# Performance work log

Hardware: AMD Instinct MI355X
Metric: run time of the kernel (lower is better)

## Reference

```python
import jax, jax.numpy as jnp
import numpy as np
from jax import lax

S, B, IN, H, L = 256, 8192, 1, 32, 2


def setup_inputs() -> dict:
    key = jax.random.key(0)
    ks = jax.random.split(key, 12)
    s = 1.0 / np.sqrt(H)
    return {
        "x": jax.random.normal(ks[0], (S, B, IN), dtype=jnp.float32),
        "h": jax.random.normal(ks[1], (L, B, H), dtype=jnp.float32),
        "W_ih0": jax.random.uniform(ks[2], (3 * H, IN), jnp.float32, -s, s),
        "W_hh0": jax.random.uniform(ks[3], (3 * H, H), jnp.float32, -s, s),
        "b_ih0": jax.random.uniform(ks[4], (3 * H,), jnp.float32, -s, s),
        "b_hh0": jax.random.uniform(ks[5], (3 * H,), jnp.float32, -s, s),
        "W_ih1": jax.random.uniform(ks[6], (3 * H, H), jnp.float32, -s, s),
        "W_hh1": jax.random.uniform(ks[7], (3 * H, H), jnp.float32, -s, s),
        "b_ih1": jax.random.uniform(ks[8], (3 * H,), jnp.float32, -s, s),
        "b_hh1": jax.random.uniform(ks[9], (3 * H,), jnp.float32, -s, s),
        "W_out": jax.random.uniform(ks[10], (1, H), jnp.float32, -s, s),
        "b_out": jax.random.uniform(ks[11], (1,), jnp.float32, -s, s),
    }


def _gru_layer(x_seq, h0, W_ih, W_hh, b_ih, b_hh):
    # x_seq: (S, B, D_in), h0: (B, H). PyTorch GRU gate math.
    def step(h, x_t):
        gi = x_t @ W_ih.T + b_ih            # (B, 3H)
        gh = h @ W_hh.T + b_hh              # (B, 3H)
        i_r, i_z, i_n = jnp.split(gi, 3, axis=-1)
        h_r, h_z, h_n = jnp.split(gh, 3, axis=-1)
        r = jax.nn.sigmoid(i_r + h_r)
        z = jax.nn.sigmoid(i_z + h_z)
        n = jnp.tanh(i_n + r * h_n)
        h_new = (1.0 - z) * n + z * h
        return h_new, h_new

    h_last, out = lax.scan(step, h0, x_seq)
    return out, h_last


def reference(x, h, W_ih0, W_hh0, b_ih0, b_hh0, W_ih1, W_hh1, b_ih1, b_hh1, W_out, b_out):
    out0, hl0 = _gru_layer(x, h[0], W_ih0, W_hh0, b_ih0, b_hh0)
    out1, hl1 = _gru_layer(out0, h[1], W_ih1, W_hh1, b_ih1, b_hh1)
    # per-timestep Linear loop == one batched matmul over (S, B, H)
    y = out1 @ W_out.T + b_out              # (S, B, 1)
    h_state = jnp.stack([hl0, hl1], axis=0)  # (L, B, H)
    return (y, h_state)
```

## Files before the change

kernel.cpp:

```cpp
#include <hip/hip_runtime.h>


#define S_LEN 256
#define B_SZ  8192
#define H_SZ  32
#define RS    40

typedef __attribute__((ext_vector_type(8))) short short8;
typedef __attribute__((ext_vector_type(4))) float f32x4;

#define MFMA(a, b, c) __builtin_amdgcn_mfma_f32_16x16x32_bf16(a, b, c, 0, 0, 0)

#if __has_builtin(__builtin_amdgcn_exp2f)
#define EXP2F(x) __builtin_amdgcn_exp2f(x)
#else
#define EXP2F(x) exp2f(x)
#endif
#if __has_builtin(__builtin_amdgcn_rcpf)
#define RCPF(x) __builtin_amdgcn_rcpf(x)
#else
#define RCPF(x) (1.0f / (x))
#endif

__device__ __forceinline__ float sigm_pre(float p) {
    return RCPF(1.0f + EXP2F(p));
}
__device__ __forceinline__ float tanh_pre(float p) {
    return 1.0f - 2.0f * RCPF(1.0f + EXP2F(p));
}

__device__ __forceinline__ unsigned short bf_rne1(float f) {
    union { float f; unsigned u; } x; x.f = f;
    unsigned u = x.u + 0x7fffu + ((x.u >> 16) & 1u);
    return (unsigned short)(u >> 16);
}

#if __has_builtin(__builtin_amdgcn_cvt_pk_bf16_f32)
typedef __bf16 bf16x2 __attribute__((ext_vector_type(2)));
__device__ __forceinline__ unsigned pk2(float a, float b) {
    union { bf16x2 v; unsigned u; } c;
    c.v = __builtin_amdgcn_cvt_pk_bf16_f32(a, b);
    return c.u;
}
#else
__device__ __forceinline__ unsigned pk2(float a, float b) {
    return (unsigned)bf_rne1(a) | ((unsigned)bf_rne1(b) << 16);
}
#endif

union Frag { short8 s8; unsigned u[4]; };

__global__ __launch_bounds__(256) void gru_bf(
    const float* __restrict__ x,
    const float* __restrict__ h_in,
    const float* __restrict__ W_ih0,
    const float* __restrict__ W_hh0,
    const float* __restrict__ b_ih0,
    const float* __restrict__ b_hh0,
    const float* __restrict__ W_ih1,
    const float* __restrict__ W_hh1,
    const float* __restrict__ b_ih1,
    const float* __restrict__ b_hh1,
    const float* __restrict__ W_out,
    const float* __restrict__ b_out,
    float* __restrict__ out)
{
    __shared__ __align__(16) float sx[S_LEN * 16];
    __shared__ __align__(16) float sy[2][S_LEN * 16];
    __shared__ __align__(16) unsigned short sh0s[3][16 * RS];
    __shared__ __align__(16) unsigned short sh1s[3][16 * RS];

    const int tid  = threadIdx.x;
    const int w    = tid >> 6;
    const int lane = tid & 63;
    const int n    = lane & 15;
    const int q    = lane >> 4;
    const int base = blockIdx.x * 16;
    const int bn   = base + n;
    const int wl   = w & 1;

    for (int s = tid; s < S_LEN * 4; s += 256) {
        const int t = s >> 2, c = s & 3;
        *(float4*)&sx[t * 16 + c * 4] = *(const float4*)&x[t * B_SZ + base + c * 4];
    }

    const float SRZ = -1.4426950408889634f;
    const float SN  =  2.8853900817779268f;

    short8 A_h[3], A_i[3];
    f32x4  C_h[3], C_i3;
    float  wi0r[4], wi0z[4], wi0n[4], bi0n[4];
    float  wo[4];
    float  hd[4];

    if (w < 2) {
#pragma unroll
        for (int t = 0; t < 3; ++t) {
            const float sc = (t < 2) ? SRZ : SN;
            const int row = 32 * t + 16 * wl + n;
#pragma unroll
            for (int e = 0; e < 8; ++e)
                A_h[t][e] = (short)bf_rne1(W_hh0[row * H_SZ + q * 8 + e] * sc);
#pragma unroll
            for (int r = 0; r < 4; ++r) {
                const int g = 32 * t + 16 * wl + 4 * q + r;
                C_h[t][r] = (t < 2) ? SRZ * (b_ih0[g] + b_hh0[g])
                                    : SN * b_hh0[g];
            }
        }
#pragma unroll
        for (int r = 0; r < 4; ++r) {
            const int j = 16 * wl + 4 * q + r;
            wi0r[r] = SRZ * W_ih0[j];
            wi0z[r] = SRZ * W_ih0[32 + j];
            wi0n[r] = SN  * W_ih0[64 + j];
            bi0n[r] = SN  * b_ih0[64 + j];
            hd[r]   = h_in[bn * H_SZ + j];
            wo[r]   = 0.f;
        }
    } else {
#pragma unroll
        for (int t = 0; t < 3; ++t) {
            const float sc = (t < 2) ? SRZ : SN;
            const int row = 32 * t + 16 * wl + n;
#pragma unroll
            for (int e = 0; e < 8; ++e) {
                A_h[t][e] = (short)bf_rne1(W_hh1[row * H_SZ + q * 8 + e] * sc);
                A_i[t][e] = (short)bf_rne1(W_ih1[row * H_SZ + q * 8 + e] * sc);
            }
#pragma unroll
            for (int r = 0; r < 4; ++r) {
                const int g = 32 * t + 16 * wl + 4 * q + r;
                C_h[t][r] = (t < 2) ? SRZ * (b_ih1[g] + b_hh1[g])
                                    : SN * b_hh1[g];
                if (t == 2) C_i3[r] = SN * b_ih1[g];
            }
        }
#pragma unroll
        for (int r = 0; r < 4; ++r) {
            const int j = 16 * wl + 4 * q + r;
            hd[r] = h_in[B_SZ * H_SZ + bn * H_SZ + j];
            wo[r] = W_out[j];
        }
    }
    const f32x4 Z4 = {0.f, 0.f, 0.f, 0.f};
    const float bout = b_out[0];

    short8 B0, B1;
    {
        Frag f;
        const float4 a = *(const float4*)&h_in[bn * H_SZ + q * 8];
        const float4 b = *(const float4*)&h_in[bn * H_SZ + q * 8 + 4];
        f.u[0] = pk2(a.x, a.y); f.u[1] = pk2(a.z, a.w);
        f.u[2] = pk2(b.x, b.y); f.u[3] = pk2(b.z, b.w);
        B0 = f.s8;
        const float4 c = *(const float4*)&h_in[B_SZ * H_SZ + bn * H_SZ + q * 8];
        const float4 d = *(const float4*)&h_in[B_SZ * H_SZ + bn * H_SZ + q * 8 + 4];
        f.u[0] = pk2(c.x, c.y); f.u[1] = pk2(c.z, c.w);
        f.u[2] = pk2(d.x, d.y); f.u[3] = pk2(d.z, d.w);
        B1 = f.s8;
    }

    __syncthreads();

    int buf = 0;
#pragma unroll 1
    for (int i = 0; i <= S_LEN; ++i) {
        if (w < 2) {
            if (i < S_LEN) {
                const float xc = sx[i * 16 + n];
                const f32x4 g0r = MFMA(A_h[0], B0, C_h[0]);
                const f32x4 g0z = MFMA(A_h[1], B0, C_h[1]);
                const f32x4 g0n = MFMA(A_h[2], B0, C_h[2]);
                float hv4[4];
#pragma unroll
                for (int r = 0; r < 4; ++r) {
                    const float rg = sigm_pre(fmaf(xc, wi0r[r], g0r[r]));
                    const float zg = sigm_pre(fmaf(xc, wi0z[r], g0z[r]));
                    const float ng = tanh_pre(fmaf(rg, g0n[r],
                                                   fmaf(xc, wi0n[r], bi0n[r])));
                    const float hv = fmaf(zg, hd[r] - ng, ng);
                    hd[r] = hv;
                    hv4[r] = hv;
                }
                *(uint2*)&sh0s[buf][n * RS + 16 * wl + 4 * q] =
                    make_uint2(pk2(hv4[0], hv4[1]), pk2(hv4[2], hv4[3]));
            }
        } else {
            if (i > 0) {
                const f32x4 ur = MFMA(A_h[0], B1, C_h[0]);
                const f32x4 uz = MFMA(A_h[1], B1, C_h[1]);
                const f32x4 un = MFMA(A_h[2], B1, C_h[2]);
                const f32x4 vr = MFMA(A_i[0], B0, Z4);
                const f32x4 vz = MFMA(A_i[1], B0, Z4);
                const f32x4 vn = MFMA(A_i[2], B0, C_i3);
                float hv4[4];
                float ys = 0.f;
#pragma unroll
                for (int r = 0; r < 4; ++r) {
                    const float rg = sigm_pre(ur[r] + vr[r]);
                    const float zg = sigm_pre(uz[r] + vz[r]);
                    const float ng = tanh_pre(fmaf(rg, un[r], vn[r]));
                    const float hv = fmaf(zg, hd[r] - ng, ng);
                    hd[r] = hv;
                    hv4[r] = hv;
                    ys = fmaf(hv, wo[r], ys);
                }
                *(uint2*)&sh1s[buf][n * RS + 16 * wl + 4 * q] =
                    make_uint2(pk2(hv4[0], hv4[1]), pk2(hv4[2], hv4[3]));
                ys += __shfl_xor(ys, 16);
                ys += __shfl_xor(ys, 32);
                if (lane < 16) sy[wl][(i - 1) * 16 + n] = ys;
            }
        }

        __syncthreads();

        if (i < S_LEN)
            B0 = *(const short8*)&sh0s[buf][n * RS + q * 8];
        if (w >= 2 && i > 0)
            B1 = *(const short8*)&sh1s[buf][n * RS + q * 8];

        buf = (buf == 2) ? 0 : buf + 1;
    }

    __syncthreads();

    for (int s = tid; s < S_LEN * 4; s += 256) {
        const int t = s >> 2, c = s & 3;
        const float4 a = *(const float4*)&sy[0][t * 16 + c * 4];
        const float4 b = *(const float4*)&sy[1][t * 16 + c * 4];
        *(float4*)&out[t * B_SZ + base + c * 4] =
            make_float4(a.x + b.x + bout, a.y + b.y + bout,
                        a.z + b.z + bout, a.w + b.w + bout);
    }

    const int j = 16 * wl + 4 * q;
    if (w < 2)
        *(float4*)&out[S_LEN * B_SZ + bn * H_SZ + j] =
            make_float4(hd[0], hd[1], hd[2], hd[3]);
    else
        *(float4*)&out[S_LEN * B_SZ + B_SZ * H_SZ + bn * H_SZ + j] =
            make_float4(hd[0], hd[1], hd[2], hd[3]);
}

extern "C" void kernel_launch(void* const* d_in, const int* in_sizes, int n_in,
                              void* d_out, int out_size, void* d_ws, size_t ws_size,
                              hipStream_t stream) {
    (void)in_sizes; (void)n_in; (void)out_size; (void)d_ws; (void)ws_size;
    const float* x     = (const float*)d_in[0];
    const float* h_in  = (const float*)d_in[1];
    const float* W_ih0 = (const float*)d_in[2];
    const float* W_hh0 = (const float*)d_in[3];
    const float* b_ih0 = (const float*)d_in[4];
    const float* b_hh0 = (const float*)d_in[5];
    const float* W_ih1 = (const float*)d_in[6];
    const float* W_hh1 = (const float*)d_in[7];
    const float* b_ih1 = (const float*)d_in[8];
    const float* b_hh1 = (const float*)d_in[9];
    const float* W_out = (const float*)d_in[10];
    const float* b_out = (const float*)d_in[11];

    dim3 grid(B_SZ / 16);
    dim3 block(256);
    gru_bf<<<grid, block, 0, stream>>>(x, h_in, W_ih0, W_hh0, b_ih0, b_hh0,
                                       W_ih1, W_hh1, b_ih1, b_hh1,
                                       W_out, b_out, (float*)d_out);
}
```

Before: 269.0 us.

## Double-buffer hidden state and compute output projection from shared bf16 state

```diff
diff --git a/kernel.cpp b/kernel.cpp
--- a/kernel.cpp
+++ b/kernel.cpp
@@ -48,9 +48,11 @@
 }
 #endif
 
-union Frag { short8 s8; unsigned u[4]; };
-
-__global__ __launch_bounds__(256) void gru_bf(
+__device__ __forceinline__ float bits_f(unsigned u) {
+    union { unsigned u; float f; } x; x.u = u; return x.f;
+}
+
+__global__ __launch_bounds__(256) void gru_lag(
     const float* __restrict__ x,
     const float* __restrict__ h_in,
     const float* __restrict__ W_ih0,
@@ -65,10 +67,10 @@
     const float* __restrict__ b_out,
     float* __restrict__ out)
 {
+    __shared__ __align__(16) unsigned short sh0[2][16 * RS];
+    __shared__ __align__(16) unsigned short sh1[2][16 * RS];
     __shared__ __align__(16) float sx[S_LEN * 16];
-    __shared__ __align__(16) float sy[2][S_LEN * 16];
-    __shared__ __align__(16) unsigned short sh0s[3][16 * RS];
-    __shared__ __align__(16) unsigned short sh1s[3][16 * RS];
+    __shared__ __align__(16) float sy[S_LEN * 16];
 
     const int tid  = threadIdx.x;
     const int w    = tid >> 6;
@@ -90,7 +92,7 @@
     short8 A_h[3], A_i[3];
     f32x4  C_h[3], C_i3;
     float  wi0r[4], wi0z[4], wi0n[4], bi0n[4];
-    float  wo[4];
+    float  wo8[8];
     float  hd[4];
 
     if (w < 2) {
@@ -116,7 +118,6 @@
             wi0n[r] = SN  * W_ih0[64 + j];
             bi0n[r] = SN  * b_ih0[64 + j];
             hd[r]   = h_in[bn * H_SZ + j];
-            wo[r]   = 0.f;
         }
     } else {
 #pragma unroll
@@ -137,111 +138,119 @@
             }
         }
 #pragma unroll
-        for (int r = 0; r < 4; ++r) {
-            const int j = 16 * wl + 4 * q + r;
-            hd[r] = h_in[B_SZ * H_SZ + bn * H_SZ + j];
-            wo[r] = W_out[j];
-        }
+        for (int r = 0; r < 4; ++r)
+            hd[r] = h_in[B_SZ * H_SZ + bn * H_SZ + 16 * wl + 4 * q + r];
+#pragma unroll
+        for (int e = 0; e < 8; ++e) wo8[e] = W_out[q * 8 + e];
     }
     const f32x4 Z4 = {0.f, 0.f, 0.f, 0.f};
     const float bout = b_out[0];
 
     short8 B0, B1;
     {
-        Frag f;
-        const float4 a = *(const float4*)&h_in[bn * H_SZ + q * 8];
-        const float4 b = *(const float4*)&h_in[bn * H_SZ + q * 8 + 4];
+        const float* hsrc = h_in + (size_t)(w >= 2) * B_SZ * H_SZ + bn * H_SZ + q * 8;
+        union { short8 s8; unsigned u[4]; } f;
+        const float4 a = *(const float4*)&hsrc[0];
+        const float4 b = *(const float4*)&hsrc[4];
         f.u[0] = pk2(a.x, a.y); f.u[1] = pk2(a.z, a.w);
         f.u[2] = pk2(b.x, b.y); f.u[3] = pk2(b.z, b.w);
-        B0 = f.s8;
-        const float4 c = *(const float4*)&h_in[B_SZ * H_SZ + bn * H_SZ + q * 8];
-        const float4 d = *(const float4*)&h_in[B_SZ * H_SZ + bn * H_SZ + q * 8 + 4];
-        f.u[0] = pk2(c.x, c.y); f.u[1] = pk2(c.z, c.w);
-        f.u[2] = pk2(d.x, d.y); f.u[3] = pk2(d.z, d.w);
-        B1 = f.s8;
-    }
+        if (w < 2) B0 = f.s8; else B1 = f.s8;
+    }
+
+    const int wroff = n * RS + 16 * wl + 4 * q;
+    const int rdoff = n * RS + 8 * q;
 
     __syncthreads();
-
-    int buf = 0;
-#pragma unroll 1
+    float xcur = (w < 2) ? sx[n] : 0.0f;
+
+#pragma unroll 2
     for (int i = 0; i <= S_LEN; ++i) {
+        const int buf = i & 1;
         if (w < 2) {
             if (i < S_LEN) {
-                const float xc = sx[i * 16 + n];
-                const f32x4 g0r = MFMA(A_h[0], B0, C_h[0]);
-                const f32x4 g0z = MFMA(A_h[1], B0, C_h[1]);
-                const f32x4 g0n = MFMA(A_h[2], B0, C_h[2]);
+                const f32x4 Dr = MFMA(A_h[0], B0, C_h[0]);
+                const f32x4 Dz = MFMA(A_h[1], B0, C_h[1]);
+                const f32x4 Dn = MFMA(A_h[2], B0, C_h[2]);
                 float hv4[4];
 #pragma unroll
                 for (int r = 0; r < 4; ++r) {
-                    const float rg = sigm_pre(fmaf(xc, wi0r[r], g0r[r]));
-                    const float zg = sigm_pre(fmaf(xc, wi0z[r], g0z[r]));
-                    const float ng = tanh_pre(fmaf(rg, g0n[r],
-                                                   fmaf(xc, wi0n[r], bi0n[r])));
-                    const float hv = fmaf(zg, hd[r] - ng, ng);
-                    hd[r] = hv;
-                    hv4[r] = hv;
+                    const float rg = sigm_pre(fmaf(xcur, wi0r[r], Dr[r]));
+                    const float zg = sigm_pre(fmaf(xcur, wi0z[r], Dz[r]));
+                    const float ng = tanh_pre(fmaf(rg, Dn[r],
+                                                   fmaf(xcur, wi0n[r], bi0n[r])));
+                    const float v = fmaf(zg, hd[r] - ng, ng);
+                    hd[r] = v;
+                    hv4[r] = v;
                 }
-                *(uint2*)&sh0s[buf][n * RS + 16 * wl + 4 * q] =
+                *(uint2*)&sh0[buf][wroff] =
                     make_uint2(pk2(hv4[0], hv4[1]), pk2(hv4[2], hv4[3]));
             }
         } else {
             if (i > 0) {
-                const f32x4 ur = MFMA(A_h[0], B1, C_h[0]);
-                const f32x4 uz = MFMA(A_h[1], B1, C_h[1]);
-                const f32x4 un = MFMA(A_h[2], B1, C_h[2]);
-                const f32x4 vr = MFMA(A_i[0], B0, Z4);
-                const f32x4 vz = MFMA(A_i[1], B0, Z4);
-                const f32x4 vn = MFMA(A_i[2], B0, C_i3);
+                const f32x4 Ur = MFMA(A_h[0], B1, C_h[0]);
+                const f32x4 Uz = MFMA(A_h[1], B1, C_h[1]);
+                const f32x4 Un = MFMA(A_h[2], B1, C_h[2]);
+                const f32x4 Vr = MFMA(A_i[0], B0, Z4);
+                const f32x4 Vz = MFMA(A_i[1], B0, Z4);
+                const f32x4 Vn = MFMA(A_i[2], B0, C_i3);
                 float hv4[4];
-                float ys = 0.f;
 #pragma unroll
                 for (int r = 0; r < 4; ++r) {
-                    const float rg = sigm_pre(ur[r] + vr[r]);
-                    const float zg = sigm_pre(uz[r] + vz[r]);
-                    const float ng = tanh_pre(fmaf(rg, un[r], vn[r]));
-                    const float hv = fmaf(zg, hd[r] - ng, ng);
-                    hd[r] = hv;
-                    hv4[r] = hv;
-                    ys = fmaf(hv, wo[r], ys);
+                    const float rg = sigm_pre(Ur[r] + Vr[r]);
+                    const float zg = sigm_pre(Uz[r] + Vz[r]);
+                    const float ng = tanh_pre(fmaf(rg, Un[r], Vn[r]));
+                    const float v = fmaf(zg, hd[r] - ng, ng);
+                    hd[r] = v;
+                    hv4[r] = v;
                 }
-                *(uint2*)&sh1s[buf][n * RS + 16 * wl + 4 * q] =
+                *(uint2*)&sh1[buf][wroff] =
                     make_uint2(pk2(hv4[0], hv4[1]), pk2(hv4[2], hv4[3]));
-                ys += __shfl_xor(ys, 16);
-                ys += __shfl_xor(ys, 32);
-                if (lane < 16) sy[wl][(i - 1) * 16 + n] = ys;
             }
         }
 
         __syncthreads();
 
-        if (i < S_LEN)
-            B0 = *(const short8*)&sh0s[buf][n * RS + q * 8];
-        if (w >= 2 && i > 0)
-            B1 = *(const short8*)&sh1s[buf][n * RS + q * 8];
-
-        buf = (buf == 2) ? 0 : buf + 1;
+        if (w < 2) {
+            if (i < S_LEN) {
+                B0 = *(const short8*)&sh0[buf][rdoff];
+                const int tn = (i + 1 < S_LEN) ? i + 1 : i;
+                xcur = sx[tn * 16 + n];
+            }
+        } else {
+            if (i < S_LEN)
+                B0 = *(const short8*)&sh0[buf][rdoff];
+            if (i > 0) {
+                B1 = *(const short8*)&sh1[buf][rdoff];
+                if (w == 2) {
+                    union { short8 s8; unsigned u[4]; } f; f.s8 = B1;
+                    float ys = bits_f(f.u[0] << 16) * wo8[0];
+                    ys = fmaf(bits_f(f.u[0] & 0xffff0000u), wo8[1], ys);
+                    ys = fmaf(bits_f(f.u[1] << 16),         wo8[2], ys);
+                    ys = fmaf(bits_f(f.u[1] & 0xffff0000u), wo8[3], ys);
+                    ys = fmaf(bits_f(f.u[2] << 16),         wo8[4], ys);
+                    ys = fmaf(bits_f(f.u[2] & 0xffff0000u), wo8[5], ys);
+                    ys = fmaf(bits_f(f.u[3] << 16),         wo8[6], ys);
+                    ys = fmaf(bits_f(f.u[3] & 0xffff0000u), wo8[7], ys);
+                    ys += __shfl_xor(ys, 16);
+                    ys += __shfl_xor(ys, 32);
+                    if (lane < 16) sy[(i - 1) * 16 + n] = ys;
+                }
+            }
+        }
     }
 
     __syncthreads();
 
     for (int s = tid; s < S_LEN * 4; s += 256) {
         const int t = s >> 2, c = s & 3;
-        const float4 a = *(const float4*)&sy[0][t * 16 + c * 4];
-        const float4 b = *(const float4*)&sy[1][t * 16 + c * 4];
+        const float4 a = *(const float4*)&sy[t * 16 + c * 4];
         *(float4*)&out[t * B_SZ + base + c * 4] =
-            make_float4(a.x + b.x + bout, a.y + b.y + bout,
-                        a.z + b.z + bout, a.w + b.w + bout);
-    }
-
-    const int j = 16 * wl + 4 * q;
-    if (w < 2)
-        *(float4*)&out[S_LEN * B_SZ + bn * H_SZ + j] =
-            make_float4(hd[0], hd[1], hd[2], hd[3]);
-    else
-        *(float4*)&out[S_LEN * B_SZ + B_SZ * H_SZ + bn * H_SZ + j] =
-            make_float4(hd[0], hd[1], hd[2], hd[3]);
+            make_float4(a.x + bout, a.y + bout, a.z + bout, a.w + bout);
+    }
+
+    const size_t hoff = (size_t)S_LEN * B_SZ + (size_t)(w >= 2) * B_SZ * H_SZ;
+    *(float4*)&out[hoff + bn * H_SZ + 16 * wl + 4 * q] =
+        make_float4(hd[0], hd[1], hd[2], hd[3]);
 }
 
 extern "C" void kernel_launch(void* const* d_in, const int* in_sizes, int n_in,
@@ -263,7 +272,7 @@
 
     dim3 grid(B_SZ / 16);
     dim3 block(256);
-    gru_bf<<<grid, block, 0, stream>>>(x, h_in, W_ih0, W_hh0, b_ih0, b_hh0,
-                                       W_ih1, W_hh1, b_ih1, b_hh1,
-                                       W_out, b_out, (float*)d_out);
-}
+    gru_lag<<<grid, block, 0, stream>>>(x, h_in, W_ih0, W_hh0, b_ih0, b_hh0,
+                                        W_ih1, W_hh1, b_ih1, b_hh1,
+                                        W_out, b_out, (float*)d_out);
+}
```

Result: no change. 267.3 us (-0.6%).
